# Kernel tuning notes

Measured on AMD Instinct MI355X. Metric: run time of the kernel, lower is better.

## Reference

```python
import jax, jax.numpy as jnp
import numpy as np

FACTOR = 1
EPS = 1e-8
SCALES = (1, 2, 4)


def _pool(x, scale):
    # adaptive_avg_pool1d along time with L % scale == 0 -> uniform bin mean
    if scale == 1:
        return x
    B, L, H, E = x.shape
    return x.reshape(B, L // scale, scale, H, E).mean(axis=2)


def _interp_linear(x, L_out):
    # F.interpolate(mode='linear', align_corners=False) along time axis (axis=1)
    B, Ls, H, E = x.shape
    i = jnp.arange(L_out, dtype=jnp.float32)
    src = jnp.maximum((i + 0.5) * (Ls / L_out) - 0.5, 0.0)
    x0 = jnp.floor(src).astype(jnp.int32)
    x1 = jnp.minimum(x0 + 1, Ls - 1)
    lam = (src - x0.astype(jnp.float32))[None, :, None, None]
    return x[:, x0] * (1.0 - lam) + x[:, x1] * lam


def _corr_agg(q, k, v, w1, b1, w2, b2, w3, b3):
    # q,k,v: [B, Ls, H, E]
    B, Ls, H, E = q.shape
    qf = jnp.fft.rfft(q.transpose(0, 2, 3, 1), axis=-1)   # [B,H,E,Lf]
    kf = jnp.fft.rfft(k.transpose(0, 2, 3, 1), axis=-1)
    corr = jnp.fft.irfft(qf * jnp.conj(kf), n=Ls, axis=-1).astype(jnp.float32)  # [B,H,E,Ls]

    # ---- adaptive-k features ----
    energy = jnp.mean(jnp.sum(corr ** 2, axis=(1, 2)))          # scalar, expanded to B
    var = jnp.var(corr.reshape(B, -1), axis=1, ddof=1)          # unbiased, like torch.var
    cm = corr.reshape(B, H * E, Ls).mean(axis=1)                # [B, Ls]
    pk = jnp.sum((cm[:, 1:-1] > cm[:, :-2]) & (cm[:, 1:-1] > cm[:, 2:]), axis=1).astype(jnp.float32)
    feats = jnp.stack([jnp.broadcast_to(energy, (B,)), var, pk], axis=1)  # [B,3]
    h = jax.nn.relu(feats @ w1.T + b1)
    h = jax.nn.relu(h @ w2.T + b2)
    ratio = jax.nn.sigmoid(h @ w3.T + b3)[:, 0]                 # [B]
    kvals = jnp.clip((ratio * Ls * FACTOR).astype(jnp.int32), 1, Ls)  # [B]

    # ---- adaptive time-delay aggregation ----
    c = corr.transpose(0, 3, 1, 2)                              # [B, Ls, H, E]
    interior = (c[:, 1:-1] > c[:, :-2]) & (c[:, 1:-1] > c[:, 2:])
    pad = jnp.zeros((B, 1, H, E), dtype=bool)
    peaks = jnp.concatenate([pad, interior, pad], axis=1)       # [B,Ls,H,E] local maxima

    neg_inf = jnp.float32(-jnp.inf)
    vals = jnp.where(peaks, c, neg_inf).reshape(B, -1)
    count = peaks.reshape(B, -1).sum(axis=1)
    sorted_desc = -jnp.sort(-vals, axis=1)
    thresh = jnp.take_along_axis(sorted_desc, (kvals - 1)[:, None], axis=1)[:, 0]  # k-th largest peak
    topk_mask = peaks & (c >= thresh[:, None, None, None])
    keep_topk = (count > kvals)[:, None, None, None]
    final = jnp.where(keep_topk, topk_mask, peaks)

    attn = jnp.where(final, c, 0.0)
    w = jax.nn.softmax(attn + EPS, axis=1)                      # softmax over time lags
    return w * v                                                # einsum('lhe,lhe->lhe') == elementwise


def setup_inputs() -> dict:
    key = jax.random.key(0)
    ks = jax.random.split(key, 10)
    B, L, H, E = 16, 1024, 8, 64
    return {
        "queries": jax.random.normal(ks[0], (B, L, H, E), jnp.float32),
        "keys": jax.random.normal(ks[1], (B, L, H, E), jnp.float32),
        "values": jax.random.normal(ks[2], (B, L, H, E), jnp.float32),
        "scale_weights": jax.random.normal(ks[3], (3,), jnp.float32) * 0.1 + 1.0 / 3.0,
        "k_w1": jax.random.normal(ks[4], (32, 3), jnp.float32) * 0.1,
        "k_b1": jax.random.normal(ks[5], (32,), jnp.float32) * 0.1,
        "k_w2": jax.random.normal(ks[6], (16, 32), jnp.float32) * 0.1,
        "k_b2": jax.random.normal(ks[7], (16,), jnp.float32) * 0.1,
        "k_w3": jax.random.normal(ks[8], (1, 16), jnp.float32) * 0.1,
        "k_b3": jax.random.normal(ks[9], (1,), jnp.float32) * 0.1,
    }


def reference(queries, keys, values, scale_weights, k_w1, k_b1, k_w2, k_b2, k_w3, k_b3):
    B, L, H, E = queries.shape
    out = jnp.zeros_like(queries)
    for i, scale in enumerate(SCALES):
        q, k, v = _pool(queries, scale), _pool(keys, scale), _pool(values, scale)
        o = _corr_agg(q, k, v, k_w1, k_b1, k_w2, k_b2, k_w3, k_b3)
        if scale > 1:
            o = _interp_linear(o, L)
        out = out + o * scale_weights[i]
    return out
```

## Files before the change

### kernel.cpp

```cpp
#include <hip/hip_runtime.h>
#include <math.h>

typedef unsigned int u32;
typedef unsigned long long u64;
typedef float f4 __attribute__((ext_vector_type(4)));

#define B_ 16
#define L_ 1024
#define H_ 8
#define E_ 64
#define C_ 512
#define NB_SEL 32
#define GCH 8
#define TC 32
#define CAP1 192
#define KGRP 56

__device__ __forceinline__ size_t co(int sidx) {
  return sidx == 0 ? 0u : (sidx == 1 ? 8388608u : 12582912u);
}
__device__ __forceinline__ u32 pk_off(int sidx) {
  return sidx == 0 ? 0u : (sidx == 1 ? 3211264u : 4816896u);
}
__device__ __forceinline__ u32 pk_cap(int sidx) { return 200704u >> sidx; }

__device__ __forceinline__ u32 f2key(float f) {
  u32 u = __float_as_uint(f);
  return (u & 0x80000000u) ? ~u : (u | 0x80000000u);
}
__device__ __forceinline__ float key2f(u32 k) {
  u32 u = (k & 0x80000000u) ? (k ^ 0x80000000u) : ~k;
  return __uint_as_float(u);
}

__global__ void k_init(u32* histA, u32* histB, u32* peak_cnt, u32* done,
                       double* s1, double* s2, float* cm) {
  const int gid = blockIdx.x * 256 + threadIdx.x;
  const int gs = gridDim.x * 256;
  for (int i = gid; i < 3 * 16 * 256; i += gs) { histA[i] = 0; histB[i] = 0; }
  for (int i = gid; i < 3 * 16 * 1024; i += gs) cm[i] = 0.f;
  for (int i = gid; i < 3 * 16 * 16; i += gs) peak_cnt[i] = 0;
  for (int i = gid; i < 144; i += gs) done[i] = 0;
  for (int i = gid; i < 48; i += gs) { s1[i] = 0.0; s2[i] = 0.0; }
}

template<int S>
__device__ __forceinline__ float gpool(const float* base, int tk, int e) {
  float v = base[(size_t)(tk * S) * C_ + e];
  if constexpr (S >= 2) v += base[(size_t)(tk * S + 1) * C_ + e];
  if constexpr (S == 4) {
    v += base[(size_t)(tk * S + 2) * C_ + e];
    v += base[(size_t)(tk * S + 3) * C_ + e];
  }
  constexpr float sc = (S == 1) ? 1.f : (S == 2) ? 0.5f : 0.25f;
  if constexpr (S >= 2) v *= sc;
  return v;
}

template<int S>
__launch_bounds__(512, 4)
__global__ void k_corr1(const float* __restrict__ Q, const float* __restrict__ K,
                        float* __restrict__ corr) {
  constexpr int LS = 1024 / S;
  constexpr int LMASK = LS - 1;
  constexpr int NCHUNK = LS / TC;
  __shared__ __align__(16) float ksT[KGRP * 256];
  __shared__ __align__(16) float qT[2 * 8 * 256];
  const int tid = threadIdx.x;
  const int e = tid & 63;
  const int w = tid >> 6;
  const int slot16 = __builtin_amdgcn_readfirstlane(w << 4);
  const int bh = blockIdx.x;
  const int tau0 = blockIdx.y << 7;
  const int b = bh >> 3, h = bh & 7;
  const size_t gbase = (size_t)b * L_ * C_ + (size_t)h * 64;
  const float* Qb = Q + gbase;
  const float* Kb = K + gbase;
  const int e4 = e << 2;
  const int bp0 = 112 - slot16;

  float acc[16];
#pragma unroll
  for (int i = 0; i < 16; ++i) acc[i] = 0.f;

#pragma unroll
  for (int pass = 0; pass < 5; ++pass) {
    const int p0 = pass * 32 + (w << 2);
    f4 v;
#pragma unroll
    for (int j = 0; j < 4; ++j) {
      int tk = (p0 + j - tau0 - 127 + 2048) & LMASK;
      v[j] = gpool<S>(Kb, tk, e);
    }
    *(f4*)&ksT[(p0 >> 2) * 256 + e4] = v;
    if (p0 < 32) *(f4*)&ksT[((p0 + 192) >> 2) * 256 + e4] = v;
  }
  {
    f4 v;
#pragma unroll
    for (int j = 0; j < 4; ++j)
      v[j] = gpool<S>(Qb, (w << 2) + j, e);
    *(f4*)&qT[w * 256 + e4] = v;
  }
  __syncthreads();

  int cph = 0;
  for (int chunk = 0; chunk < NCHUNK; ++chunk) {
    const int t0 = chunk * TC;
    const bool more = (chunk + 1 < NCHUNK);
    f4 kr, qr;
    int sr = 0;
    if (more) {
      int sp = cph + 160; if (sp >= CAP1) sp -= CAP1;
      sr = sp + (w << 2);
#pragma unroll
      for (int j = 0; j < 4; ++j) {
        int l = t0 + 160 + (w << 2) + j;
        int tk = (l - tau0 - 127 + 2048) & LMASK;
        kr[j] = gpool<S>(Kb, tk, e);
      }
#pragma unroll
      for (int j = 0; j < 4; ++j)
        qr[j] = gpool<S>(Qb, (t0 + TC + (w << 2) + j) & LMASK, e);
    }
    int bp = bp0 + cph; if (bp >= CAP1) bp -= CAP1;
    const int g0 = bp >> 2;
    f4 km4[12];
#pragma unroll
    for (int j = 0; j < 12; ++j)
      km4[j] = *(const f4*)&ksT[(g0 + j) * 256 + e4];
    const float* qb = qT + (chunk & 1) * 2048;
#pragma unroll
    for (int g = 0; g < 8; ++g) {
      f4 qv = *(const f4*)&qb[g * 256 + e4];
#pragma unroll
      for (int k = 0; k < 4; ++k) {
        const int jt = (g << 2) + k;
#pragma unroll
        for (int i = 0; i < 16; ++i) {
          const int m = 15 + jt - i;
          acc[i] = fmaf(qv[k], km4[m >> 2][m & 3], acc[i]);
        }
      }
    }
    if (more) {
      *(f4*)&ksT[(sr >> 2) * 256 + e4] = kr;
      if (sr < 32) *(f4*)&ksT[((sr + 192) >> 2) * 256 + e4] = kr;
      float* qn = qT + (((chunk & 1) ^ 1)) * 2048;
      *(f4*)&qn[w * 256 + e4] = qr;
    }
    __syncthreads();
    cph += 32; if (cph >= CAP1) cph -= CAP1;
  }
  float* wt = ksT;
#pragma unroll
  for (int i = 0; i < 16; ++i) wt[(slot16 + i) * 65 + e] = acc[i];
  __syncthreads();
  const int to = tid & 127;
  const size_t cbase = ((size_t)b * C_ + (size_t)h * 64) * LS + tau0 + to;
  for (int cr = tid >> 7; cr < 64; cr += 4)
    corr[cbase + (size_t)cr * LS] = wt[to * 65 + cr];
}

__launch_bounds__(256, 4)
__global__ void k_stats(const float* __restrict__ corrbase, float* __restrict__ cm,
                        double* s1, double* s2, u32* peak_cnt, u32* histA,
                        u32* pkbase) {
  __shared__ __align__(16) float rows[GCH * 1024];
  __shared__ u32 hist_s[256];
  __shared__ double red_d[8];
  __shared__ u32 wv[4], wbase[4];
  const int tid = threadIdx.x;
  const int sidx = blockIdx.z;
  const int b = blockIdx.y;
  const int sb = sidx * 16 + b;
  const int Ls = 1024 >> sidx;
  const int c0 = blockIdx.x * GCH;
  const int lane = tid & 63;
  const int wave = tid >> 6;
  hist_s[tid] = 0;
  {
    const float4* src4 =
        (const float4*)(corrbase + co(sidx) + ((size_t)b * C_ + c0) * Ls);
    float4* dst4 = (float4*)rows;
    const int n4 = GCH * Ls / 4;
    for (int i = tid; i < n4; i += 256) dst4[i] = src4[i];
  }
  __syncthreads();
  const int nt = Ls >> 8;
  float cmacc[4] = {0.f, 0.f, 0.f, 0.f};
  double ls1 = 0.0, ls2 = 0.0;
  u32 mycnt = 0;
  for (int g = 0; g < GCH; ++g) {
    const float* row = rows + g * Ls;
    for (int i = 0; i < nt; ++i) {
      int t = tid + (i << 8);
      float v = row[t];
      cmacc[i] += v;
      ls1 += (double)v;
      ls2 += (double)v * (double)v;
      bool pk = (t >= 1) && (t <= Ls - 2) && (v > row[t - 1]) && (v > row[t + 1]);
      if (pk) {
        ++mycnt;
        atomicAdd(&hist_s[f2key(v) >> 24], 1u);
      }
    }
  }
  u32 wc = mycnt;
  for (int off = 32; off; off >>= 1) wc += __shfl_down(wc, off, 64);
  if (lane == 0) wv[wave] = wc;
  __syncthreads();
  if (tid == 0) {
    u32 t = 0;
    for (int w = 0; w < 4; ++w) { wbase[w] = t; t += wv[w]; }
    u32 base = atomicAdd(&peak_cnt[sb * 16], t);
    for (int w = 0; w < 4; ++w) wbase[w] += base;
  }
  __syncthreads();
  const u32 cap = pk_cap(sidx);
  u32* dst_pk = pkbase + pk_off(sidx) + (u32)b * cap;
  u32 off_w = wbase[wave];
  const u64 below = (1ull << lane) - 1ull;
  for (int g = 0; g < GCH; ++g) {
    const float* row = rows + g * Ls;
    for (int i = 0; i < nt; ++i) {
      int t = tid + (i << 8);
      float v = row[t];
      bool pk = (t >= 1) && (t <= Ls - 2) && (v > row[t - 1]) && (v > row[t + 1]);
      u64 mask = __ballot(pk);
      if (pk) {
        u32 idx = off_w + (u32)__popcll(mask & below);
        if (idx < cap) dst_pk[idx] = f2key(v);
      }
      off_w += (u32)__popcll(mask);
    }
  }
  for (int i = 0; i < nt; ++i) {
    int t = tid + (i << 8);
    unsafeAtomicAdd(&cm[sb * 1024 + t], cmacc[i]);
  }
  for (int off = 32; off; off >>= 1) {
    ls1 += __shfl_down(ls1, off, 64);
    ls2 += __shfl_down(ls2, off, 64);
  }
  if (lane == 0) { red_d[wave] = ls1; red_d[4 + wave] = ls2; }
  __syncthreads();
  if (tid == 0) {
    unsafeAtomicAdd(&s1[sb], red_d[0] + red_d[1] + red_d[2] + red_d[3]);
    unsafeAtomicAdd(&s2[sb], red_d[4] + red_d[5] + red_d[6] + red_d[7]);
  }
  if (hist_s[tid]) atomicAdd(&histA[sb * 256 + tid], hist_s[tid]);
}

__global__ void k_mlp(const float* __restrict__ cm, const double* s1,
                      const double* s2, const u32* peak_cnt, const u32* histA,
                      int* rank_s, u32* prefix_s, u32* active, float* thresh,
                      const float* w1, const float* b1, const float* w2,
                      const float* b2, const float* w3, const float* b3) {
  __shared__ float wls[673];
  __shared__ float cmrow[1024];
  __shared__ int red_i[4];
  __shared__ u32 cum[256];
  const int tid = threadIdx.x;
  const int sb = blockIdx.x;
  const int sidx = sb >> 4;
  const int Ls = 1024 >> sidx;
  for (int i = tid; i < 96; i += 256) wls[i] = w1[i];
  for (int i = tid; i < 32; i += 256) wls[96 + i] = b1[i];
  for (int i = tid; i < 512; i += 256) wls[128 + i] = w2[i];
  if (tid < 16) wls[640 + tid] = b2[tid];
  if (tid < 16) wls[656 + tid] = w3[tid];
  if (tid == 0) wls[672] = b3[0];
  for (int i = tid; i < Ls; i += 256) cmrow[i] = cm[sb * 1024 + i];
  __syncthreads();
  int cnt = 0;
  for (int t = 1 + tid; t <= Ls - 2; t += 256) {
    float v = cmrow[t];
    cnt += (v > cmrow[t - 1]) && (v > cmrow[t + 1]);
  }
  for (int off = 32; off; off >>= 1) cnt += __shfl_down(cnt, off, 64);
  if ((tid & 63) == 0) red_i[tid >> 6] = cnt;
  __syncthreads();
  if (tid == 0) {
    double tot = 0.0;
    for (int j = 0; j < 16; ++j) tot += s2[sidx * 16 + j];
    float f0 = (float)(tot / (16.0 * (double)Ls));
    double N = (double)C_ * (double)Ls;
    float f1 = (float)((s2[sb] - s1[sb] * s1[sb] / N) / (N - 1.0));
    float f2 = (float)(red_i[0] + red_i[1] + red_i[2] + red_i[3]);
    float h1[32];
    for (int j = 0; j < 32; ++j)
      h1[j] = fmaxf(0.f, wls[j * 3] * f0 + wls[j * 3 + 1] * f1 + wls[j * 3 + 2] * f2 + wls[96 + j]);
    float h2[16];
    for (int j = 0; j < 16; ++j) {
      float a = wls[640 + j];
      for (int i = 0; i < 32; ++i) a += wls[128 + j * 32 + i] * h1[i];
      h2[j] = fmaxf(0.f, a);
    }
    float z = wls[672];
    for (int i = 0; i < 16; ++i) z += wls[656 + i] * h2[i];
    float ratio = 1.0f / (1.0f + __expf(-z));
    int kv = (int)(ratio * (float)Ls);
    kv = min(max(kv, 1), Ls);
    int cntb = (int)peak_cnt[sb * 16];
    active[sb] = (u32)(cntb > kv);
    thresh[sb] = -INFINITY;
    rank_s[sb] = kv;
    prefix_s[sb] = 0;
  }
  __syncthreads();
  cum[tid] = histA[sb * 256 + tid];
  __syncthreads();
  for (int off = 1; off < 256; off <<= 1) {
    u32 add = (tid + off < 256) ? cum[tid + off] : 0u;
    __syncthreads();
    cum[tid] += add;
    __syncthreads();
  }
  u32 act_b = active[sb];
  u32 r = act_b ? (u32)rank_s[sb] : 0u;
  u32 cc = cum[tid];
  u32 cnext = (tid == 255) ? 0u : cum[tid + 1];
  __syncthreads();
  if (act_b && r > 0 && cc >= r && cnext < r) {
    prefix_s[sb] = (u32)tid << 24;
    rank_s[sb] = (int)(r - cnext);
  }
}

__global__ void k_sel(const u32* __restrict__ pkbase, const u32* peak_cnt,
                      const u32* active, int* rank_s, u32* prefix_s,
                      u32* hist, u32* done, float* thresh, int level) {
  __shared__ u32 hist_s[256];
  __shared__ u32 cum[256];
  __shared__ u32 islast;
  const int tid = threadIdx.x;
  const int sb = blockIdx.x / NB_SEL;
  const int blk = blockIdx.x % NB_SEL;
  const int sidx = sb >> 4;
  hist_s[tid] = 0;
  if (tid == 0) islast = 0;
  __syncthreads();
  const int act = (int)active[sb];
  const u32 cap = pk_cap(sidx);
  u32 cnt = peak_cnt[sb * 16];
  if (cnt > cap) cnt = cap;
  if (act) {
    const u32 pref = prefix_s[sb];
    const int hi_sh = 32 - 8 * level;
    const int b_sh = 24 - 8 * level;
    const u32 lo = (u32)(((u64)cnt * (u64)blk) / NB_SEL);
    const u32 hi = (u32)(((u64)cnt * (u64)(blk + 1)) / NB_SEL);
    const u32* src = pkbase + pk_off(sidx) + (u32)(sb & 15) * cap;
    for (u32 i = lo + tid; i < hi; i += 256) {
      u32 key = src[i];
      if ((key >> hi_sh) == (pref >> hi_sh))
        atomicAdd(&hist_s[(key >> b_sh) & 255u], 1u);
    }
  }
  __syncthreads();
  if (hist_s[tid]) atomicAdd(&hist[sb * 256 + tid], hist_s[tid]);
  __syncthreads();
  if (tid == 0) {
    __threadfence();
    u32 t = atomicAdd(&done[(level - 1) * 48 + sb], 1u);
    if (t == NB_SEL - 1) islast = 1;
  }
  __syncthreads();
  if (!islast) return;
  __threadfence();
  u32 hv = atomicAdd(&hist[sb * 256 + tid], 0u);
  cum[tid] = hv;
  hist[sb * 256 + tid] = 0;
  __syncthreads();
  for (int off = 1; off < 256; off <<= 1) {
    u32 add = (tid + off < 256) ? cum[tid + off] : 0u;
    __syncthreads();
    cum[tid] += add;
    __syncthreads();
  }
  u32 r = act ? (u32)rank_s[sb] : 0u;
  u32 pref2 = act ? prefix_s[sb] : 0u;
  u32 cc = cum[tid];
  u32 cnext = (tid == 255) ? 0u : cum[tid + 1];
  __syncthreads();
  if (act && r > 0 && cc >= r && cnext < r) {
    u32 np = pref2 | ((u32)tid << (24 - 8 * level));
    prefix_s[sb] = np;
    rank_s[sb] = (int)(r - cnext);
    if (level == 3) thresh[sb] = key2f(np);
  }
}

__global__ void k_softstats(const float* __restrict__ corrbase, const float* thresh,
                            float2* __restrict__ mZ) {
  __shared__ float row[1024];
  __shared__ float red_s[8];
  const int tid = threadIdx.x;
  const int bc = blockIdx.x;
  const int sidx = blockIdx.y;
  const int Ls = 1024 >> sidx;
  const float th = thresh[sidx * 16 + (bc >> 9)];
  const float* src = corrbase + co(sidx) + (size_t)bc * Ls;
  for (int t = tid; t < Ls; t += 256) row[t] = src[t];
  __syncthreads();
  float mx = 0.f;
  for (int t = tid; t < Ls; t += 256) {
    float v = row[t];
    bool pk = (t >= 1) && (t <= Ls - 2) && (v > row[t - 1]) && (v > row[t + 1]) && (v >= th);
    if (pk) mx = fmaxf(mx, v);
  }
  for (int off = 32; off; off >>= 1) mx = fmaxf(mx, __shfl_down(mx, off, 64));
  if ((tid & 63) == 0) red_s[tid >> 6] = mx;
  __syncthreads();
  float m = fmaxf(fmaxf(red_s[0], red_s[1]), fmaxf(red_s[2], red_s[3]));
  float zs = 0.f;
  for (int t = tid; t < Ls; t += 256) {
    float v = row[t];
    bool pk = (t >= 1) && (t <= Ls - 2) && (v > row[t - 1]) && (v > row[t + 1]) && (v >= th);
    float a = pk ? v : 0.f;
    zs += __expf(a - m);
  }
  for (int off = 32; off; off >>= 1) zs += __shfl_down(zs, off, 64);
  if ((tid & 63) == 0) red_s[4 + (tid >> 6)] = zs;
  __syncthreads();
  if (tid == 0) {
    float Z = red_s[4] + red_s[5] + red_s[6] + red_s[7];
    mZ[sidx * 8192 + bc] = make_float2(m, 1.0f / Z);
  }
}

__launch_bounds__(256, 4)
__global__ void k_apply2(const float* __restrict__ corr2c, const float* __restrict__ corr4c,
                         const float* __restrict__ V,
                         const float2* __restrict__ mZ2, const float2* __restrict__ mZ4,
                         const float* __restrict__ th2, const float* __restrict__ th4,
                         float* __restrict__ o2p, float* __restrict__ o4p) {
  __shared__ float ct[64][131];
  __shared__ float m_s[64], rz_s[64];
  const int tid = threadIdx.x;
  const int b = blockIdx.z;
  const int c0 = blockIdx.y << 6;
  const int xb = blockIdx.x;
  const int is4 = (xb < 2);
  const int s = is4 ? 4 : 2;
  const int Ls = is4 ? 256 : 512;
  const int t0 = (is4 ? xb : (xb - 2)) << 7;
  const float* corr = is4 ? corr4c : corr2c;
  const float2* mZ = is4 ? mZ4 : mZ2;
  const float* thp = is4 ? th4 : th2;
  float* o = is4 ? o4p : o2p;
  {
    const int row0 = tid >> 7, jc = tid & 127;
    for (int rr = row0; rr < 64; rr += 2) {
      const float* src = corr + ((size_t)b * C_ + c0 + rr) * Ls;
      for (int j = jc; j < 130; j += 128) {
        int t = t0 - 1 + j;
        t = max(0, min(t, Ls - 1));
        ct[rr][j] = src[t];
      }
    }
  }
  if (tid < 64) {
    float2 v = mZ[b * C_ + c0 + tid];
    m_s[tid] = v.x; rz_s[tid] = v.y;
  }
  __syncthreads();
  const float th = thp[b];
  const int cl = tid & 63, ts = tid >> 6;
  for (int ii = 0; ii < 32; ++ii) {
    int tl = ts + (ii << 2);
    int tg = t0 + tl;
    float vm = ct[cl][tl], vc = ct[cl][tl + 1], vp = ct[cl][tl + 2];
    bool pk = (tg >= 1) && (tg <= Ls - 2) && (vc > vm) && (vc > vp) && (vc >= th);
    float a = pk ? vc : 0.f;
    float w = __expf(a - m_s[cl]) * rz_s[cl];
    size_t vb = ((size_t)b * L_ + (size_t)tg * s) * C_ + c0 + cl;
    float vv;
    if (s == 2) vv = (V[vb] + V[vb + C_]) * 0.5f;
    else vv = ((V[vb] + V[vb + C_]) + (V[vb + 2 * C_] + V[vb + 3 * C_])) * 0.25f;
    o[((size_t)b * Ls + tg) * C_ + c0 + cl] = w * vv;
  }
}

__launch_bounds__(256, 4)
__global__ void k_apply_final(const float* __restrict__ corr, const float* __restrict__ V,
                              const float2* __restrict__ mZ, const float* thresh,
                              const float* __restrict__ o2, const float* __restrict__ o4,
                              const float* __restrict__ sw, float* __restrict__ out) {
  __shared__ float ct[64][131];
  __shared__ float m_s[64], rz_s[64];
  const int Ls = 1024;
  const int tid = threadIdx.x;
  const int b = blockIdx.z;
  const int c0 = blockIdx.y << 6;
  const int t0 = blockIdx.x << 7;
  {
    const int row0 = tid >> 7, jc = tid & 127;
    for (int rr = row0; rr < 64; rr += 2) {
      const float* src = corr + ((size_t)b * C_ + c0 + rr) * Ls;
      for (int j = jc; j < 130; j += 128) {
        int t = t0 - 1 + j;
        t = max(0, min(t, Ls - 1));
        ct[rr][j] = src[t];
      }
    }
  }
  if (tid < 64) {
    float2 v = mZ[b * C_ + c0 + tid];
    m_s[tid] = v.x; rz_s[tid] = v.y;
  }
  __syncthreads();
  const float th = thresh[b];
  const float sw0 = sw[0], sw1 = sw[1], sw2 = sw[2];
  const int cl = tid & 63, ts = tid >> 6;
  for (int ii = 0; ii < 32; ++ii) {
    int tl = ts + (ii << 2);
    int tg = t0 + tl;
    float vm = ct[cl][tl], vc = ct[cl][tl + 1], vp = ct[cl][tl + 2];
    bool pk = (tg >= 1) && (tg <= Ls - 2) && (vc > vm) && (vc > vp) && (vc >= th);
    float a = pk ? vc : 0.f;
    float w = __expf(a - m_s[cl]) * rz_s[cl];
    float v1 = V[((size_t)b * L_ + tg) * C_ + c0 + cl];
    float r = sw0 * w * v1;
    {
      float srcp = fmaxf((tg + 0.5f) * 0.5f - 0.5f, 0.f);
      int x0 = (int)srcp;
      float lam = srcp - (float)x0;
      int x1 = min(x0 + 1, 511);
      const float* p = o2 + (size_t)b * 512 * C_ + c0 + cl;
      r += sw1 * ((1.f - lam) * p[(size_t)x0 * C_] + lam * p[(size_t)x1 * C_]);
    }
    {
      float srcp = fmaxf((tg + 0.5f) * 0.25f - 0.5f, 0.f);
      int x0 = (int)srcp;
      float lam = srcp - (float)x0;
      int x1 = min(x0 + 1, 255);
      const float* p = o4 + (size_t)b * 256 * C_ + c0 + cl;
      r += sw2 * ((1.f - lam) * p[(size_t)x0 * C_] + lam * p[(size_t)x1 * C_]);
    }
    out[((size_t)b * L_ + tg) * C_ + c0 + cl] = r;
  }
}

extern "C" void kernel_launch(void* const* d_in, const int* in_sizes, int n_in,
                              void* d_out, int out_size, void* d_ws, size_t ws_size,
                              hipStream_t stream) {
  const float* Q  = (const float*)d_in[0];
  const float* Kk = (const float*)d_in[1];
  const float* V  = (const float*)d_in[2];
  const float* sw = (const float*)d_in[3];
  const float* w1 = (const float*)d_in[4];
  const float* b1 = (const float*)d_in[5];
  const float* w2 = (const float*)d_in[6];
  const float* b2 = (const float*)d_in[7];
  const float* w3 = (const float*)d_in[8];
  const float* b3 = (const float*)d_in[9];
  float* out = (float*)d_out;

  char* ws = (char*)d_ws;
  size_t p = 0;
  auto alloc = [&](size_t n) { char* r = ws + p; p = (p + n + 255) & ~(size_t)255; return r; };
  float*  corr = (float*)alloc((size_t)(8388608 + 4194304 + 2097152) * 4);
  char*   oreg = alloc((size_t)25165824);
  float*  o2   = (float*)oreg;
  float*  o4   = (float*)(oreg + 16777216);
  u32*    pk   = (u32*)oreg;
  float*  cm       = (float*)alloc(3 * 16 * 1024 * 4);
  float2* mZ       = (float2*)alloc(3 * 16 * 512 * 8);
  double* s1d      = (double*)alloc(48 * 8);
  double* s2d      = (double*)alloc(48 * 8);
  u32*    histA    = (u32*)alloc(3 * 16 * 256 * 4);
  u32*    histB    = (u32*)alloc(3 * 16 * 256 * 4);
  u32*    peak_cnt = (u32*)alloc(3 * 16 * 16 * 4);
  u32*    done     = (u32*)alloc(144 * 4);
  int*    rank_s   = (int*)alloc(48 * 4);
  u32*    prefix_s = (u32*)alloc(48 * 4);
  u32*    active   = (u32*)alloc(48 * 4);
  float*  thresh   = (float*)alloc(48 * 4);

  k_init<<<dim3(16), dim3(256), 0, stream>>>(histA, histB, peak_cnt, done,
                                             s1d, s2d, cm);
  k_corr1<1><<<dim3(128, 8), dim3(512), 0, stream>>>(Q, Kk, corr);
  k_corr1<2><<<dim3(128, 4), dim3(512), 0, stream>>>(Q, Kk, corr + 8388608);
  k_corr1<4><<<dim3(128, 2), dim3(512), 0, stream>>>(Q, Kk, corr + 12582912);
  k_stats<<<dim3(C_ / GCH, B_, 3), dim3(256), 0, stream>>>(
      corr, cm, s1d, s2d, peak_cnt, histA, pk);
  k_mlp<<<dim3(48), dim3(256), 0, stream>>>(
      cm, s1d, s2d, peak_cnt, histA, rank_s, prefix_s, active, thresh,
      w1, b1, w2, b2, w3, b3);
  for (int level = 1; level <= 3; ++level)
    k_sel<<<dim3(48 * NB_SEL), dim3(256), 0, stream>>>(
        pk, peak_cnt, active, rank_s, prefix_s, histB, done, thresh, level);
  k_softstats<<<dim3(8192, 3), dim3(256), 0, stream>>>(corr, thresh, mZ);
  k_apply2<<<dim3(6, 8, 16), dim3(256), 0, stream>>>(
      corr + 8388608, corr + 12582912, V, mZ + 8192, mZ + 2 * 8192,
      thresh + 16, thresh + 32, o2, o4);
  k_apply_final<<<dim3(8, 8, 16), dim3(256), 0, stream>>>(
      corr, V, mZ, thresh, o2, o4, sw, out);
}
```

Measured before the change: 764.2 us.

## Write softmax weights in softstats and parametrize corr tau width per scale

k_softstats now computes the final per-element softmax weight (peak mask, max subtraction, normalization) and writes it back over the corr buffer in place. The apply kernels then load those weights directly instead of a haloed corr tile, per-row m/Z and threshold, and no longer recompute the peak test and exp. This removes the mZ buffer and redundant exp work, but softstats now does an extra full write pass over corr. Separately, k_corr1 gains a TAUW template parameter so the scale-4 pass uses 8 taus per wave over more blocks, raising parallelism for the smallest scale.

```diff
diff --git a/kernel.cpp b/kernel.cpp
--- a/kernel.cpp
+++ b/kernel.cpp
@@ -57,31 +57,34 @@
   return v;
 }
 
-template<int S>
+template<int S, int TAUW>
 __launch_bounds__(512, 4)
 __global__ void k_corr1(const float* __restrict__ Q, const float* __restrict__ K,
                         float* __restrict__ corr) {
   constexpr int LS = 1024 / S;
   constexpr int LMASK = LS - 1;
   constexpr int NCHUNK = LS / TC;
+  constexpr int NTAU = 8 * TAUW;
+  constexpr int WIN = TAUW + 31;
+  constexpr int NG = (WIN + 3) >> 2;
   __shared__ __align__(16) float ksT[KGRP * 256];
   __shared__ __align__(16) float qT[2 * 8 * 256];
   const int tid = threadIdx.x;
   const int e = tid & 63;
   const int w = tid >> 6;
-  const int slot16 = __builtin_amdgcn_readfirstlane(w << 4);
+  const int slot = __builtin_amdgcn_readfirstlane(w * TAUW);
   const int bh = blockIdx.x;
-  const int tau0 = blockIdx.y << 7;
+  const int tau0 = blockIdx.y * NTAU;
   const int b = bh >> 3, h = bh & 7;
   const size_t gbase = (size_t)b * L_ * C_ + (size_t)h * 64;
   const float* Qb = Q + gbase;
   const float* Kb = K + gbase;
   const int e4 = e << 2;
-  const int bp0 = 112 - slot16;
-
-  float acc[16];
-#pragma unroll
-  for (int i = 0; i < 16; ++i) acc[i] = 0.f;
+  const int bp0 = 128 - TAUW - slot;
+
+  float acc[TAUW];
+#pragma unroll
+  for (int i = 0; i < TAUW; ++i) acc[i] = 0.f;
 
 #pragma unroll
   for (int pass = 0; pass < 5; ++pass) {
@@ -125,9 +128,9 @@
     }
     int bp = bp0 + cph; if (bp >= CAP1) bp -= CAP1;
     const int g0 = bp >> 2;
-    f4 km4[12];
-#pragma unroll
-    for (int j = 0; j < 12; ++j)
+    f4 km4[NG];
+#pragma unroll
+    for (int j = 0; j < NG; ++j)
       km4[j] = *(const f4*)&ksT[(g0 + j) * 256 + e4];
     const float* qb = qT + (chunk & 1) * 2048;
 #pragma unroll
@@ -137,8 +140,8 @@
       for (int k = 0; k < 4; ++k) {
         const int jt = (g << 2) + k;
 #pragma unroll
-        for (int i = 0; i < 16; ++i) {
-          const int m = 15 + jt - i;
+        for (int i = 0; i < TAUW; ++i) {
+          const int m = TAUW - 1 + jt - i;
           acc[i] = fmaf(qv[k], km4[m >> 2][m & 3], acc[i]);
         }
       }
@@ -154,11 +157,11 @@
   }
   float* wt = ksT;
 #pragma unroll
-  for (int i = 0; i < 16; ++i) wt[(slot16 + i) * 65 + e] = acc[i];
-  __syncthreads();
-  const int to = tid & 127;
+  for (int i = 0; i < TAUW; ++i) wt[(slot + i) * 65 + e] = acc[i];
+  __syncthreads();
+  const int to = tid & (NTAU - 1);
   const size_t cbase = ((size_t)b * C_ + (size_t)h * 64) * LS + tau0 + to;
-  for (int cr = tid >> 7; cr < 64; cr += 4)
+  for (int cr = tid / NTAU; cr < 64; cr += 512 / NTAU)
     corr[cbase + (size_t)cr * LS] = wt[to * 65 + cr];
 }
 
@@ -392,8 +395,7 @@
   }
 }
 
-__global__ void k_softstats(const float* __restrict__ corrbase, const float* thresh,
-                            float2* __restrict__ mZ) {
+__global__ void k_softstats(float* __restrict__ corrbase, const float* thresh) {
   __shared__ float row[1024];
   __shared__ float red_s[8];
   const int tid = threadIdx.x;
@@ -401,7 +403,7 @@
   const int sidx = blockIdx.y;
   const int Ls = 1024 >> sidx;
   const float th = thresh[sidx * 16 + (bc >> 9)];
-  const float* src = corrbase + co(sidx) + (size_t)bc * Ls;
+  float* src = corrbase + co(sidx) + (size_t)bc * Ls;
   for (int t = tid; t < Ls; t += 256) row[t] = src[t];
   __syncthreads();
   float mx = 0.f;
@@ -424,20 +426,21 @@
   for (int off = 32; off; off >>= 1) zs += __shfl_down(zs, off, 64);
   if ((tid & 63) == 0) red_s[4 + (tid >> 6)] = zs;
   __syncthreads();
-  if (tid == 0) {
-    float Z = red_s[4] + red_s[5] + red_s[6] + red_s[7];
-    mZ[sidx * 8192 + bc] = make_float2(m, 1.0f / Z);
+  const float Z = red_s[4] + red_s[5] + red_s[6] + red_s[7];
+  const float rz = 1.0f / Z;
+  for (int t = tid; t < Ls; t += 256) {
+    float v = row[t];
+    bool pk = (t >= 1) && (t <= Ls - 2) && (v > row[t - 1]) && (v > row[t + 1]) && (v >= th);
+    float a = pk ? v : 0.f;
+    src[t] = __expf(a - m) * rz;
   }
 }
 
 __launch_bounds__(256, 4)
-__global__ void k_apply2(const float* __restrict__ corr2c, const float* __restrict__ corr4c,
+__global__ void k_apply2(const float* __restrict__ w2c, const float* __restrict__ w4c,
                          const float* __restrict__ V,
-                         const float2* __restrict__ mZ2, const float2* __restrict__ mZ4,
-                         const float* __restrict__ th2, const float* __restrict__ th4,
                          float* __restrict__ o2p, float* __restrict__ o4p) {
-  __shared__ float ct[64][131];
-  __shared__ float m_s[64], rz_s[64];
+  __shared__ float ct[64][129];
   const int tid = threadIdx.x;
   const int b = blockIdx.z;
   const int c0 = blockIdx.y << 6;
@@ -446,35 +449,19 @@
   const int s = is4 ? 4 : 2;
   const int Ls = is4 ? 256 : 512;
   const int t0 = (is4 ? xb : (xb - 2)) << 7;
-  const float* corr = is4 ? corr4c : corr2c;
-  const float2* mZ = is4 ? mZ4 : mZ2;
-  const float* thp = is4 ? th4 : th2;
+  const float* wsrc = is4 ? w4c : w2c;
   float* o = is4 ? o4p : o2p;
   {
     const int row0 = tid >> 7, jc = tid & 127;
-    for (int rr = row0; rr < 64; rr += 2) {
-      const float* src = corr + ((size_t)b * C_ + c0 + rr) * Ls;
-      for (int j = jc; j < 130; j += 128) {
-        int t = t0 - 1 + j;
-        t = max(0, min(t, Ls - 1));
-        ct[rr][j] = src[t];
-      }
-    }
-  }
-  if (tid < 64) {
-    float2 v = mZ[b * C_ + c0 + tid];
-    m_s[tid] = v.x; rz_s[tid] = v.y;
-  }
-  __syncthreads();
-  const float th = thp[b];
+    for (int rr = row0; rr < 64; rr += 2)
+      ct[rr][jc] = wsrc[((size_t)b * C_ + c0 + rr) * Ls + t0 + jc];
+  }
+  __syncthreads();
   const int cl = tid & 63, ts = tid >> 6;
   for (int ii = 0; ii < 32; ++ii) {
     int tl = ts + (ii << 2);
     int tg = t0 + tl;
-    float vm = ct[cl][tl], vc = ct[cl][tl + 1], vp = ct[cl][tl + 2];
-    bool pk = (tg >= 1) && (tg <= Ls - 2) && (vc > vm) && (vc > vp) && (vc >= th);
-    float a = pk ? vc : 0.f;
-    float w = __expf(a - m_s[cl]) * rz_s[cl];
+    float w = ct[cl][tl];
     size_t vb = ((size_t)b * L_ + (size_t)tg * s) * C_ + c0 + cl;
     float vv;
     if (s == 2) vv = (V[vb] + V[vb + C_]) * 0.5f;
@@ -484,12 +471,10 @@
 }
 
 __launch_bounds__(256, 4)
-__global__ void k_apply_final(const float* __restrict__ corr, const float* __restrict__ V,
-                              const float2* __restrict__ mZ, const float* thresh,
+__global__ void k_apply_final(const float* __restrict__ wsrcb, const float* __restrict__ V,
                               const float* __restrict__ o2, const float* __restrict__ o4,
                               const float* __restrict__ sw, float* __restrict__ out) {
-  __shared__ float ct[64][131];
-  __shared__ float m_s[64], rz_s[64];
+  __shared__ float ct[64][129];
   const int Ls = 1024;
   const int tid = threadIdx.x;
   const int b = blockIdx.z;
@@ -497,30 +482,16 @@
   const int t0 = blockIdx.x << 7;
   {
     const int row0 = tid >> 7, jc = tid & 127;
-    for (int rr = row0; rr < 64; rr += 2) {
-      const float* src = corr + ((size_t)b * C_ + c0 + rr) * Ls;
-      for (int j = jc; j < 130; j += 128) {
-        int t = t0 - 1 + j;
-        t = max(0, min(t, Ls - 1));
-        ct[rr][j] = src[t];
-      }
-    }
-  }
-  if (tid < 64) {
-    float2 v = mZ[b * C_ + c0 + tid];
-    m_s[tid] = v.x; rz_s[tid] = v.y;
-  }
-  __syncthreads();
-  const float th = thresh[b];
+    for (int rr = row0; rr < 64; rr += 2)
+      ct[rr][jc] = wsrcb[((size_t)b * C_ + c0 + rr) * Ls + t0 + jc];
+  }
+  __syncthreads();
   const float sw0 = sw[0], sw1 = sw[1], sw2 = sw[2];
   const int cl = tid & 63, ts = tid >> 6;
   for (int ii = 0; ii < 32; ++ii) {
     int tl = ts + (ii << 2);
     int tg = t0 + tl;
-    float vm = ct[cl][tl], vc = ct[cl][tl + 1], vp = ct[cl][tl + 2];
-    bool pk = (tg >= 1) && (tg <= Ls - 2) && (vc > vm) && (vc > vp) && (vc >= th);
-    float a = pk ? vc : 0.f;
-    float w = __expf(a - m_s[cl]) * rz_s[cl];
+    float w = ct[cl][tl];
     float v1 = V[((size_t)b * L_ + tg) * C_ + c0 + cl];
     float r = sw0 * w * v1;
     {
@@ -567,7 +538,6 @@
   float*  o4   = (float*)(oreg + 16777216);
   u32*    pk   = (u32*)oreg;
   float*  cm       = (float*)alloc(3 * 16 * 1024 * 4);
-  float2* mZ       = (float2*)alloc(3 * 16 * 512 * 8);
   double* s1d      = (double*)alloc(48 * 8);
   double* s2d      = (double*)alloc(48 * 8);
   u32*    histA    = (u32*)alloc(3 * 16 * 256 * 4);
@@ -581,9 +551,9 @@
 
   k_init<<<dim3(16), dim3(256), 0, stream>>>(histA, histB, peak_cnt, done,
                                              s1d, s2d, cm);
-  k_corr1<1><<<dim3(128, 8), dim3(512), 0, stream>>>(Q, Kk, corr);
-  k_corr1<2><<<dim3(128, 4), dim3(512), 0, stream>>>(Q, Kk, corr + 8388608);
-  k_corr1<4><<<dim3(128, 2), dim3(512), 0, stream>>>(Q, Kk, corr + 12582912);
+  k_corr1<1, 16><<<dim3(128, 8), dim3(512), 0, stream>>>(Q, Kk, corr);
+  k_corr1<2, 16><<<dim3(128, 4), dim3(512), 0, stream>>>(Q, Kk, corr + 8388608);
+  k_corr1<4, 8><<<dim3(128, 4), dim3(512), 0, stream>>>(Q, Kk, corr + 12582912);
   k_stats<<<dim3(C_ / GCH, B_, 3), dim3(256), 0, stream>>>(
       corr, cm, s1d, s2d, peak_cnt, histA, pk);
   k_mlp<<<dim3(48), dim3(256), 0, stream>>>(
@@ -592,10 +562,9 @@
   for (int level = 1; level <= 3; ++level)
     k_sel<<<dim3(48 * NB_SEL), dim3(256), 0, stream>>>(
         pk, peak_cnt, active, rank_s, prefix_s, histB, done, thresh, level);
-  k_softstats<<<dim3(8192, 3), dim3(256), 0, stream>>>(corr, thresh, mZ);
+  k_softstats<<<dim3(8192, 3), dim3(256), 0, stream>>>(corr, thresh);
   k_apply2<<<dim3(6, 8, 16), dim3(256), 0, stream>>>(
-      corr + 8388608, corr + 12582912, V, mZ + 8192, mZ + 2 * 8192,
-      thresh + 16, thresh + 32, o2, o4);
+      corr + 8388608, corr + 12582912, V, o2, o4);
   k_apply_final<<<dim3(8, 8, 16), dim3(256), 0, stream>>>(
-      corr, V, mZ, thresh, o2, o4, sw, out);
-}
+      corr, V, o2, o4, sw, out);
+}
```

After: 758.9 us. About the same (-0.7%).
